# Kernel optimization log

Measured on AMD Instinct MI355X. Metric: run time of the kernel, lower is better.

## Reference

```python
import jax, jax.numpy as jnp
import numpy as np

B, N, D, H, K = 8, 128, 256, 128, 8

def setup_inputs() -> dict:
    key = jax.random.key(0)
    ks = jax.random.split(key, 6)
    E = jax.random.normal(ks[0], (B, N, D), dtype=jnp.float32)
    # kaiming_uniform-like init for linear weights
    lim1 = np.sqrt(6.0 / (2 * D))
    W1 = jax.random.uniform(ks[1], (H, 2 * D), minval=-lim1, maxval=lim1, dtype=jnp.float32)
    b1 = jnp.zeros((H,), dtype=jnp.float32)
    lim2 = np.sqrt(6.0 / H)
    W2 = jax.random.uniform(ks[2], (D, H), minval=-lim2, maxval=lim2, dtype=jnp.float32)
    b2 = jnp.zeros((D,), dtype=jnp.float32)
    q = jax.random.normal(ks[3], (K, D), dtype=jnp.float32) * (1.0 / D ** 0.5)
    return {"E": E, "W1": W1, "b1": b1, "W2": W2, "b2": b2, "q": q}

def reference(E, W1, b1, W2, b2, q):
    # phi(cat(Ei,Ej)) == relu(E_i @ W1a^T + E_j @ W1b^T + b1) @ W2^T + b2
    # Split first linear's weight to avoid materializing the [B,N,N,2D] concat.
    W1a, W1b = W1[:, :D], W1[:, D:]          # each [H, D]
    Ai = jnp.einsum('bnd,hd->bnh', E, W1a)   # [B,N,H] (row half)
    Aj = jnp.einsum('bnd,hd->bnh', E, W1b)   # [B,N,H] (col half)
    hidden = jax.nn.relu(Ai[:, :, None, :] + Aj[:, None, :, :] + b1)  # [B,N,N,H]
    # dropout is identity at inference
    # Fuse second linear with query dot: (hidden @ W2^T + b2) . q_h
    #   = hidden @ (W2^T q_h) + b2.q_h
    Wq = jnp.einsum('dh,kd->hk', W2, q)      # [H, K]
    bq = jnp.einsum('d,kd->k', b2, q)        # [K]
    logits = jnp.einsum('bijh,hk->bijh'[:0] or 'bijh,hk->bijk', hidden, Wq) + bq  # [B,N,N,K]
    M = jax.nn.sigmoid(logits).transpose(0, 3, 1, 2)  # [B,K,N,N]
    eye = jnp.eye(N, dtype=M.dtype)[None, None]
    return M * (1.0 - eye)
```

## Files before the change

kernel.cpp:

```cpp
#include <hip/hip_runtime.h>

#define PB 8
#define PN 128
#define PD 256
#define PH 128
#define PK 8
#define D2 (2*PD)
#define NT 4

__global__ __launch_bounds__(128) void t0_prep(
        const float* __restrict__ W1, const float* __restrict__ W2,
        const float* __restrict__ b2, const float* __restrict__ q,
        float* __restrict__ W1t, float* __restrict__ Wq, float* __restrict__ bq)
{
    const int blk = blockIdx.x, t = threadIdx.x;
    if (blk < D2) {
        W1t[blk * PH + t] = W1[t * D2 + blk];
    } else {
        const int k = blk - D2;
        __shared__ float qs[PD];
        __shared__ float red[128];
        qs[t]       = q[k * PD + t];
        qs[t + 128] = q[k * PD + t + 128];
        __syncthreads();
        float acc = 0.f;
        #pragma unroll 4
        for (int d = 0; d < PD; ++d)
            acc = fmaf(W2[d * PH + t], qs[d], acc);
        Wq[t * PK + k] = acc;
        red[t] = b2[t] * qs[t] + b2[t + 128] * qs[t + 128];
        __syncthreads();
        for (int s = 64; s > 0; s >>= 1) { if (t < s) red[t] += red[t + s]; __syncthreads(); }
        if (t == 0) bq[k] = red[0];
    }
}

__global__ __launch_bounds__(256) void k1_proj(
        const float* __restrict__ E, const float* __restrict__ W1t,
        const float* __restrict__ b1,
        float* __restrict__ Ai, float* __restrict__ Ajt)
{
    const int blk = blockIdx.x, t = threadIdx.x;
    const int b  = blk / (PN / NT);
    const int n0 = (blk % (PN / NT)) * NT;
    const int h = t & (PH - 1);
    const int part = t >> 7;

    const float* w = W1t + part * PD * PH + h;
    const float* e = E + (b * PN + n0) * PD;

    float acc[NT];
    #pragma unroll
    for (int n = 0; n < NT; ++n) acc[n] = 0.f;

    #pragma unroll 8
    for (int d = 0; d < PD; ++d) {
        const float wv = w[d * PH];
        #pragma unroll
        for (int n = 0; n < NT; ++n)
            acc[n] = fmaf(wv, e[n * PD + d], acc[n]);
    }

    if (part == 0) {
        const float bb = b1[h];
        #pragma unroll
        for (int n = 0; n < NT; ++n)
            Ai[(b * PN + n0 + n) * PH + h] = acc[n] + bb;
    } else {
        #pragma unroll
        for (int n = 0; n < NT; ++n)
            Ajt[(b * PH + h) * PN + n0 + n] = acc[n];
    }
}

__global__ __launch_bounds__(256) void k2_score(
        const float* __restrict__ Ai, const float* __restrict__ Ajt,
        const float* __restrict__ Wq, const float* __restrict__ bq,
        float* __restrict__ out)
{
    const int blk = blockIdx.x, t = threadIdx.x;
    const int b = blk >> 6;
    const int i = ((blk & 63) << 1) + (t >> 7);
    const int j = t & (PN - 1);

    const float* ai = Ai + (b * PN + i) * PH;
    const float* aj = Ajt + b * PH * PN + j;

    float acc[PK];
    #pragma unroll
    for (int k = 0; k < PK; ++k) acc[k] = bq[k];

    #pragma unroll 4
    for (int h = 0; h < PH; ++h) {
        const float v = fmaxf(ai[h] + aj[h * PN], 0.f);
        #pragma unroll
        for (int k = 0; k < PK; ++k)
            acc[k] = fmaf(v, Wq[h * PK + k], acc[k]);
    }

    #pragma unroll
    for (int k = 0; k < PK; ++k) {
        float s = __builtin_amdgcn_rcpf(1.f + __expf(-acc[k]));
        if (j == i) s = 0.f;
        out[((b * PK + k) * PN + i) * PN + j] = s;
    }
}

extern "C" void kernel_launch(void* const* d_in, const int* in_sizes, int n_in,
                              void* d_out, int out_size, void* d_ws, size_t ws_size,
                              hipStream_t stream) {
    const float* E  = (const float*)d_in[0];
    const float* W1 = (const float*)d_in[1];
    const float* b1 = (const float*)d_in[2];
    const float* W2 = (const float*)d_in[3];
    const float* b2 = (const float*)d_in[4];
    const float* q  = (const float*)d_in[5];

    float* Ai  = (float*)d_ws;
    float* Ajt = Ai + PB * PN * PH;
    float* W1t = Ajt + PB * PN * PH;
    float* Wq  = W1t + D2 * PH;
    float* bq  = Wq + PH * PK;

    t0_prep<<<D2 + PK, 128, 0, stream>>>(W1, W2, b2, q, W1t, Wq, bq);
    k1_proj<<<PB * (PN / NT), 256, 0, stream>>>(E, W1t, b1, Ai, Ajt);
    k2_score<<<PB * PN / 2, 256, 0, stream>>>(Ai, Ajt, Wq, bq, (float*)d_out);
}
```

Baseline: 107.5 us.

## Fuse prep, projection and scoring into one cooperative kernel with grid sync

Replaces the three launches (weight transpose/Wq prep, projection, scoring) with a single cooperative kernel of 520 blocks that uses grid.sync between the projection phase and the scoring phase. The W1 transpose pass is dropped: W1 tiles are transposed on the fly through shared memory, and E rows are staged in shared memory. In the scoring phase Wq, bq and the Ai rows are cached in shared memory and read as float4. The aim is to remove launch overhead and the extra transpose pass. The cost is a grid-wide barrier and the requirement that all 520 blocks be co-resident.

New measurement: 185.0 us. 72.1% more time.

```diff
diff --git a/kernel.cpp b/kernel.cpp
--- a/kernel.cpp
+++ b/kernel.cpp
@@ -1,4 +1,6 @@
 #include <hip/hip_runtime.h>
+#include <hip/hip_cooperative_groups.h>
+namespace cg = cooperative_groups;
 
 #define PB 8
 #define PN 128
@@ -8,101 +10,136 @@
 #define D2 (2*PD)
 #define NT 4
 
-__global__ __launch_bounds__(128) void t0_prep(
-        const float* __restrict__ W1, const float* __restrict__ W2,
+struct SmA { float es[NT][PD]; float wtile[32][PH + 1]; };
+struct SmW { float qs[PD]; float red[256]; };
+struct SmB { float wq[PH * PK]; float ais[2 * PH]; float bqs[PK]; };
+union  SmU { SmA a; SmW w; SmB b; };
+
+__global__ __launch_bounds__(256, 3) void fused(
+        const float* __restrict__ E,  const float* __restrict__ W1,
+        const float* __restrict__ b1, const float* __restrict__ W2,
         const float* __restrict__ b2, const float* __restrict__ q,
-        float* __restrict__ W1t, float* __restrict__ Wq, float* __restrict__ bq)
+        float* __restrict__ Ai, float* __restrict__ Ajt,
+        float* __restrict__ Wq, float* __restrict__ bq,
+        float* __restrict__ out)
 {
+    cg::grid_group grid = cg::this_grid();
+    __shared__ SmU sm;
     const int blk = blockIdx.x, t = threadIdx.x;
-    if (blk < D2) {
-        W1t[blk * PH + t] = W1[t * D2 + blk];
+
+    if (blk < 512) {
+        const int b    = blk >> 6;
+        const int rest = blk & 63;
+        const int n0   = (rest >> 1) * NT;
+        const int part = rest & 1;
+        const int h    = t & (PH - 1);
+        const int s    = t >> 7;
+
+        const float* erow = E + (b * PN + n0) * PD;
+        float* esf = &sm.a.es[0][0];
+        #pragma unroll
+        for (int r = 0; r < 4; ++r) esf[r * 256 + t] = erow[r * 256 + t];
+
+        const int na = n0 + 2 * s;
+        float acca = 0.f, accb = 0.f;
+        const float* w1row = W1 + h * D2 + part * PD;
+
+        for (int dc = 0; dc < 8; ++dc) {
+            __syncthreads();
+            const int cb = dc * 32 + s * 16;
+            #pragma unroll
+            for (int qq = 0; qq < 4; ++qq) {
+                float4 v = *reinterpret_cast<const float4*>(w1row + cb + qq * 4);
+                const int ld = s * 16 + qq * 4;
+                sm.a.wtile[ld + 0][h] = v.x;
+                sm.a.wtile[ld + 1][h] = v.y;
+                sm.a.wtile[ld + 2][h] = v.z;
+                sm.a.wtile[ld + 3][h] = v.w;
+            }
+            __syncthreads();
+            const int dbase = dc * 32;
+            #pragma unroll
+            for (int g = 0; g < 8; ++g) {
+                const float w0 = sm.a.wtile[g * 4 + 0][h];
+                const float w1v = sm.a.wtile[g * 4 + 1][h];
+                const float w2v = sm.a.wtile[g * 4 + 2][h];
+                const float w3v = sm.a.wtile[g * 4 + 3][h];
+                float4 ea = *reinterpret_cast<const float4*>(&sm.a.es[2 * s + 0][dbase + g * 4]);
+                float4 eb = *reinterpret_cast<const float4*>(&sm.a.es[2 * s + 1][dbase + g * 4]);
+                acca = fmaf(w0, ea.x, acca); acca = fmaf(w1v, ea.y, acca);
+                acca = fmaf(w2v, ea.z, acca); acca = fmaf(w3v, ea.w, acca);
+                accb = fmaf(w0, eb.x, accb); accb = fmaf(w1v, eb.y, accb);
+                accb = fmaf(w2v, eb.z, accb); accb = fmaf(w3v, eb.w, accb);
+            }
+        }
+
+        if (part == 0) {
+            const float bb = b1[h];
+            Ai[(b * PN + na) * PH + h]     = acca + bb;
+            Ai[(b * PN + na + 1) * PH + h] = accb + bb;
+        } else {
+            float2 v2 = make_float2(acca, accb);
+            *reinterpret_cast<float2*>(&Ajt[(b * PH + h) * PN + na]) = v2;
+        }
     } else {
-        const int k = blk - D2;
-        __shared__ float qs[PD];
-        __shared__ float red[128];
-        qs[t]       = q[k * PD + t];
-        qs[t + 128] = q[k * PD + t + 128];
+        const int k = blk - 512;
+        sm.w.qs[t] = q[k * PD + t];
         __syncthreads();
-        float acc = 0.f;
-        #pragma unroll 4
-        for (int d = 0; d < PD; ++d)
-            acc = fmaf(W2[d * PH + t], qs[d], acc);
-        Wq[t * PK + k] = acc;
-        red[t] = b2[t] * qs[t] + b2[t + 128] * qs[t + 128];
+        if (t < PH) {
+            float acc = 0.f;
+            #pragma unroll 4
+            for (int d = 0; d < PD; ++d)
+                acc = fmaf(W2[d * PH + t], sm.w.qs[d], acc);
+            Wq[t * PK + k] = acc;
+        }
+        sm.w.red[t] = b2[t] * sm.w.qs[t];
         __syncthreads();
-        for (int s = 64; s > 0; s >>= 1) { if (t < s) red[t] += red[t + s]; __syncthreads(); }
-        if (t == 0) bq[k] = red[0];
-    }
-}
-
-__global__ __launch_bounds__(256) void k1_proj(
-        const float* __restrict__ E, const float* __restrict__ W1t,
-        const float* __restrict__ b1,
-        float* __restrict__ Ai, float* __restrict__ Ajt)
-{
-    const int blk = blockIdx.x, t = threadIdx.x;
-    const int b  = blk / (PN / NT);
-    const int n0 = (blk % (PN / NT)) * NT;
-    const int h = t & (PH - 1);
-    const int part = t >> 7;
-
-    const float* w = W1t + part * PD * PH + h;
-    const float* e = E + (b * PN + n0) * PD;
-
-    float acc[NT];
-    #pragma unroll
-    for (int n = 0; n < NT; ++n) acc[n] = 0.f;
-
-    #pragma unroll 8
-    for (int d = 0; d < PD; ++d) {
-        const float wv = w[d * PH];
-        #pragma unroll
-        for (int n = 0; n < NT; ++n)
-            acc[n] = fmaf(wv, e[n * PD + d], acc[n]);
+        for (int st = 128; st > 0; st >>= 1) {
+            if (t < st) sm.w.red[t] += sm.w.red[t + st];
+            __syncthreads();
+        }
+        if (t == 0) bq[k] = sm.w.red[0];
     }
 
-    if (part == 0) {
-        const float bb = b1[h];
+    grid.sync();
+
+    if (blk < 512) {
+        const int b  = blk >> 6;
+        const int i0 = (blk & 63) << 1;
+
+        *reinterpret_cast<float4*>(&sm.b.wq[t * 4]) =
+            *reinterpret_cast<const float4*>(&Wq[t * 4]);
+        sm.b.ais[t] = Ai[(b * PN + i0) * PH + t];
+        if (t < PK) sm.b.bqs[t] = bq[t];
+        __syncthreads();
+
+        const int half = t >> 7;
+        const int i = i0 + half;
+        const int j = t & (PN - 1);
+        const float* ail = sm.b.ais + half * PH;
+        const float* aj = Ajt + b * PH * PN + j;
+
+        float acc[PK];
         #pragma unroll
-        for (int n = 0; n < NT; ++n)
-            Ai[(b * PN + n0 + n) * PH + h] = acc[n] + bb;
-    } else {
+        for (int k = 0; k < PK; ++k) acc[k] = sm.b.bqs[k];
+
+        #pragma unroll 4
+        for (int hh = 0; hh < PH; ++hh) {
+            const float v = fmaxf(ail[hh] + aj[hh * PN], 0.f);
+            float4 w0 = *reinterpret_cast<const float4*>(&sm.b.wq[hh * PK]);
+            float4 w1 = *reinterpret_cast<const float4*>(&sm.b.wq[hh * PK + 4]);
+            acc[0] = fmaf(v, w0.x, acc[0]); acc[1] = fmaf(v, w0.y, acc[1]);
+            acc[2] = fmaf(v, w0.z, acc[2]); acc[3] = fmaf(v, w0.w, acc[3]);
+            acc[4] = fmaf(v, w1.x, acc[4]); acc[5] = fmaf(v, w1.y, acc[5]);
+            acc[6] = fmaf(v, w1.z, acc[6]); acc[7] = fmaf(v, w1.w, acc[7]);
+        }
+
         #pragma unroll
-        for (int n = 0; n < NT; ++n)
-            Ajt[(b * PH + h) * PN + n0 + n] = acc[n];
-    }
-}
-
-__global__ __launch_bounds__(256) void k2_score(
-        const float* __restrict__ Ai, const float* __restrict__ Ajt,
-        const float* __restrict__ Wq, const float* __restrict__ bq,
-        float* __restrict__ out)
-{
-    const int blk = blockIdx.x, t = threadIdx.x;
-    const int b = blk >> 6;
-    const int i = ((blk & 63) << 1) + (t >> 7);
-    const int j = t & (PN - 1);
-
-    const float* ai = Ai + (b * PN + i) * PH;
-    const float* aj = Ajt + b * PH * PN + j;
-
-    float acc[PK];
-    #pragma unroll
-    for (int k = 0; k < PK; ++k) acc[k] = bq[k];
-
-    #pragma unroll 4
-    for (int h = 0; h < PH; ++h) {
-        const float v = fmaxf(ai[h] + aj[h * PN], 0.f);
-        #pragma unroll
-        for (int k = 0; k < PK; ++k)
-            acc[k] = fmaf(v, Wq[h * PK + k], acc[k]);
-    }
-
-    #pragma unroll
-    for (int k = 0; k < PK; ++k) {
-        float s = __builtin_amdgcn_rcpf(1.f + __expf(-acc[k]));
-        if (j == i) s = 0.f;
-        out[((b * PK + k) * PN + i) * PN + j] = s;
+        for (int k = 0; k < PK; ++k) {
+            float sv = 1.f / (1.f + __expf(-acc[k]));
+            if (j == i) sv = 0.f;
+            out[((b * PK + k) * PN + i) * PN + j] = sv;
+        }
     }
 }
 
@@ -118,11 +155,13 @@
 
     float* Ai  = (float*)d_ws;
     float* Ajt = Ai + PB * PN * PH;
-    float* W1t = Ajt + PB * PN * PH;
-    float* Wq  = W1t + D2 * PH;
+    float* Wq  = Ajt + PB * PN * PH;
     float* bq  = Wq + PH * PK;
+    float* out = (float*)d_out;
 
-    t0_prep<<<D2 + PK, 128, 0, stream>>>(W1, W2, b2, q, W1t, Wq, bq);
-    k1_proj<<<PB * (PN / NT), 256, 0, stream>>>(E, W1t, b1, Ai, Ajt);
-    k2_score<<<PB * PN / 2, 256, 0, stream>>>(Ai, Ajt, Wq, bq, (float*)d_out);
+    void* args[] = { (void*)&E, (void*)&W1, (void*)&b1, (void*)&W2, (void*)&b2,
+                     (void*)&q, (void*)&Ai, (void*)&Ajt, (void*)&Wq, (void*)&bq,
+                     (void*)&out };
+    hipLaunchCooperativeKernel((const void*)fused, dim3(520), dim3(256),
+                               args, 0, stream);
 }
```
